# Optimization experiments

Measured on AMD Instinct MI355X. Metric: run time of the kernel, lower is better.

Reference implementation:

```python
import jax, jax.numpy as jnp
import numpy as np

CHUNK = 2048  # mirrors torch.chunk(pc, len(pc)//2048) with N a multiple of 2048


def _half(src, ref):
    """Faithful to the original: for each chunk of `src`, compute the
    [M, chunk] squared-distance matrix against `ref` and take min over the
    chunk axis (dim 1), yielding an M-vector per chunk; concatenate.
    Result shape: [num_chunks * M]."""
    chunks = src.reshape(-1, CHUNK, src.shape[-1])  # [num_chunks, CHUNK, 3]

    def per_chunk(chunk):
        diff = ref[:, None, :] - chunk[None, :, :]          # [M, CHUNK, 3]
        d = jnp.square(jnp.sqrt(jnp.sum(diff * diff, -1)))  # norm(...)**2
        return jnp.min(d, axis=1)                           # [M]

    return jax.lax.map(per_chunk, chunks).reshape(-1)


def setup_inputs() -> dict:
    key = jax.random.key(0)
    k1, k2 = jax.random.split(key)
    output_pc = jax.random.normal(k1, (1, 16384, 3), dtype=jnp.float32)
    gt_pc = jax.random.normal(k2, (1, 16384, 3), dtype=jnp.float32)
    return {"output_pc": output_pc, "gt_pc": gt_pc}


def reference(output_pc, gt_pc):
    pc1 = jnp.squeeze(output_pc)  # [N, 3]
    pc2 = jnp.squeeze(gt_pc)      # [M, 3]
    dist1 = _half(pc1, pc2)       # [ (N//CHUNK) * M ]
    dist2 = _half(pc2, pc1)       # [ (M//CHUNK) * N ]
    return jnp.mean(dist1) + jnp.mean(dist2)
```

## Files before the change

### kernel.cpp

```cpp
#include <hip/hip_runtime.h>
#include <float.h>

#define CHUNK 2048
#define SUB   2048
#define MBLK  128
#define GRP   256
#define NGRP  (SUB / GRP)

typedef __attribute__((ext_vector_type(8)))  short short8;
typedef __attribute__((ext_vector_type(16))) float f32x16;

static __device__ __forceinline__ unsigned short f2bf(float f) {
    unsigned u = __float_as_uint(f);
    return (unsigned short)((u + 0x7FFFu + ((u >> 16) & 1u)) >> 16);
}
static __device__ __forceinline__ float bf2f(unsigned short s) {
    return __uint_as_float(((unsigned)s) << 16);
}

static __device__ __forceinline__ void gld16(const void* g, void* l) {
    __builtin_amdgcn_global_load_lds(
        (const __attribute__((address_space(1))) void*)g,
        (__attribute__((address_space(3))) void*)l, 16, 0, 0);
}

__global__ void pack_kernel(const float* __restrict__ p1,
                            const float* __restrict__ p2, int n1, int n2,
                            unsigned short* __restrict__ Arec,
                            unsigned short* __restrict__ Brec)
{
    int i = blockIdx.x * blockDim.x + threadIdx.x;
    if (i >= n1 + n2) return;
    const bool isA = (i < n1);
    const float* s = isA ? p1 : p2;
    const int j = isA ? i : i - n1;
    float x = s[3 * j + 0], y = s[3 * j + 1], z = s[3 * j + 2];

    short8 lo, hi;
    if (isA) {
        unsigned short hx = f2bf(x), hy = f2bf(y), hz = f2bf(z);
        unsigned short lx = f2bf(x - bf2f(hx)), ly = f2bf(y - bf2f(hy)),
                       lz = f2bf(z - bf2f(hz));
        float sp = fmaf(x, x, fmaf(y, y, z * z));
        unsigned short sh = f2bf(sp), sl = f2bf(sp - bf2f(sh));
        lo[0]=(short)hx; lo[1]=(short)hy; lo[2]=(short)hz;
        lo[3]=(short)lx; lo[4]=(short)ly; lo[5]=(short)lz;
        lo[6]=(short)hx; lo[7]=(short)hy;
        hi[0]=(short)hz; hi[1]=(short)lx; hi[2]=(short)ly; hi[3]=(short)lz;
        hi[4]=(short)sh; hi[5]=(short)sl; hi[6]=(short)0x3F80; hi[7]=(short)0x3F80;
        short8* dst = (short8*)(Arec + (size_t)j * 16);
        dst[0] = lo; dst[1] = hi;
    } else {
        float ux = -2.0f * x, uy = -2.0f * y, uz = -2.0f * z;
        unsigned short hx = f2bf(ux), hy = f2bf(uy), hz = f2bf(uz);
        unsigned short lx = f2bf(ux - bf2f(hx)), ly = f2bf(uy - bf2f(hy)),
                       lz = f2bf(uz - bf2f(hz));
        float sq = fmaf(x, x, fmaf(y, y, z * z));
        unsigned short sh = f2bf(sq), sl = f2bf(sq - bf2f(sh));
        lo[0]=(short)hx; lo[1]=(short)hy; lo[2]=(short)hz;
        lo[3]=(short)hx; lo[4]=(short)hy; lo[5]=(short)hz;
        lo[6]=(short)lx; lo[7]=(short)ly;
        hi[0]=(short)lz; hi[1]=(short)lx; hi[2]=(short)ly; hi[3]=(short)lz;
        hi[4]=(short)0x3F80; hi[5]=(short)0x3F80; hi[6]=(short)sh; hi[7]=(short)sl;
        short8* dst = (short8*)(Brec + (size_t)j * 16);
        dst[0] = lo; dst[1] = hi;
    }
}

static __device__ __forceinline__ float tourney16(float rm[16], int l31)
{
#pragma unroll
    for (int r = 0; r < 8; ++r) {
        float lo = fminf(rm[r],     __shfl_xor(rm[r],     16));
        float hi = fminf(rm[r + 8], __shfl_xor(rm[r + 8], 16));
        rm[r] = (l31 & 16) ? hi : lo;
    }
#pragma unroll
    for (int r = 0; r < 4; ++r) {
        float lo = fminf(rm[r],     __shfl_xor(rm[r],     8));
        float hi = fminf(rm[r + 4], __shfl_xor(rm[r + 4], 8));
        rm[r] = (l31 & 8) ? hi : lo;
    }
#pragma unroll
    for (int r = 0; r < 2; ++r) {
        float lo = fminf(rm[r],     __shfl_xor(rm[r],     4));
        float hi = fminf(rm[r + 2], __shfl_xor(rm[r + 2], 4));
        rm[r] = (l31 & 4) ? hi : lo;
    }
    {
        float lo = fminf(rm[0], __shfl_xor(rm[0], 2));
        float hi = fminf(rm[1], __shfl_xor(rm[1], 2));
        rm[0] = (l31 & 2) ? hi : lo;
    }
    return fminf(rm[0], __shfl_xor(rm[0], 1));
}

__global__ __launch_bounds__(256, 8)
void chamfer_mfma(const unsigned short* __restrict__ Arec,
                  const unsigned short* __restrict__ Brec,
                  float* __restrict__ bsum,
                  int n1, int n2, float s2, float s1)
{
    __shared__ alignas(16) unsigned short sb[2][GRP * 16];
    __shared__ float wred[4];

    const int dir = blockIdx.z;
    const unsigned short* __restrict__ Ap = dir ? Brec : Arec;
    const unsigned short* __restrict__ Bp = dir ? Arec : Brec;
    const float scale = dir ? s1 : s2;
    const int rows_n = dir ? n2 : n1;
    const int cols_n = dir ? n1 : n2;

    const int tid  = threadIdx.x;
    const int g    = blockIdx.x;
    const int yb   = blockIdx.y;
    const int bid  = g + gridDim.x * (yb + gridDim.y * dir);
    if (g * MBLK >= rows_n || yb * SUB >= cols_n) {
        if (tid == 0) bsum[bid] = 0.0f;
        return;
    }

    const int lane = tid & 63;
    const int w    = tid >> 6;
    const int half = lane >> 5;
    const int l31  = lane & 31;

    const int rA = g * MBLK + w * 32 + l31;
    short8 aA = *(const short8*)(Ap + (size_t)rA * 16 + half * 8);

    const char* Bbytes = (const char*)(Bp + (size_t)(yb * SUB) * 16);

    const unsigned su = (unsigned)tid ^ (((unsigned)tid >> 3) & 7u);

    float rm[16];
#pragma unroll
    for (int r = 0; r < 16; ++r) rm[r] = FLT_MAX;
    const f32x16 z16 = {0,0,0,0, 0,0,0,0, 0,0,0,0, 0,0,0,0};

    {
        const char* gp = Bbytes + su * 16;
        char* lp = (char*)&sb[0][0] + w * 1024;
        gld16(gp, lp);
        gld16(gp + 4096, lp + 4096);
    }
    __syncthreads();

    const unsigned ru = (((unsigned)(l31 * 2 + half)) ^ ((unsigned)l31 >> 2)) * 8u;

    for (int gr = 0; gr < NGRP; ++gr) {
        const int cur = gr & 1;
        if (gr + 1 < NGRP) {
            const char* gp = Bbytes + (size_t)(gr + 1) * 8192 + su * 16;
            char* lp = (char*)&sb[cur ^ 1][0] + w * 1024;
            gld16(gp, lp);
            gld16(gp + 4096, lp + 4096);
        }
        const unsigned short* lb = &sb[cur][ru];
#pragma unroll
        for (int tt = 0; tt < GRP / 32; ++tt) {
            short8 b = *(const short8*)(lb + (size_t)tt * 512);
            f32x16 d = __builtin_amdgcn_mfma_f32_32x32x16_bf16(aA, b, z16, 0, 0, 0);
#pragma unroll
            for (int r = 0; r < 16; ++r) rm[r] = fminf(rm[r], d[r]);
        }
        __syncthreads();
    }

    float v = tourney16(rm, l31);
    float c = ((l31 & 1) == 0) ? fmaxf(v, 0.0f) : 0.0f;
#pragma unroll
    for (int off = 32; off > 0; off >>= 1) c += __shfl_down(c, off);
    if (lane == 0) wred[w] = c;
    __syncthreads();
    if (tid == 0)
        bsum[bid] = (wred[0] + wred[1] + wred[2] + wred[3]) * scale;
}

__global__ __launch_bounds__(256)
void final_reduce(const float* __restrict__ bsum, float* __restrict__ out, int n)
{
    __shared__ float wred[4];
    float s = 0.0f;
    for (int i = threadIdx.x; i < n; i += 256) s += bsum[i];
#pragma unroll
    for (int off = 32; off > 0; off >>= 1) s += __shfl_down(s, off);
    const int lane = threadIdx.x & 63, w = threadIdx.x >> 6;
    if (lane == 0) wred[w] = s;
    __syncthreads();
    if (threadIdx.x == 0)
        out[0] = wred[0] + wred[1] + wred[2] + wred[3];
}

#define FB_RPT  2
#define FB_TILE (256 * FB_RPT)
__global__ __launch_bounds__(256, 2)
void chamfer_valu(const float* __restrict__ p1, const float* __restrict__ p2,
                  int n1, int n2, float* __restrict__ out)
{
    __shared__ float4 q[CHUNK];
    __shared__ float wsum[4];
    const int dir = blockIdx.z;
    const float* __restrict__ src = dir ? p2 : p1;
    const float* __restrict__ ref = dir ? p1 : p2;
    const int nsrc = dir ? n2 : n1;
    const int m    = dir ? n1 : n2;
    const int nchunks = nsrc / CHUNK;
    const int c = blockIdx.y;
    const int tile0 = blockIdx.x * FB_TILE;
    if (c >= nchunks || tile0 >= m) return;
    const float scale = 1.0f / ((float)nchunks * (float)m);
    const float* __restrict__ chunk = src + (size_t)c * CHUNK * 3;
    for (int k = threadIdx.x; k < CHUNK; k += 256) {
        float x = chunk[3*k], y = chunk[3*k+1], z = chunk[3*k+2];
        q[k] = make_float4(x, y, z, fmaf(x, x, fmaf(y, y, z * z)));
    }
    __syncthreads();
    float px[FB_RPT], py[FB_RPT], pz[FB_RPT], sp[FB_RPT], mna[FB_RPT], mnb[FB_RPT];
    bool valid[FB_RPT];
#pragma unroll
    for (int r = 0; r < FB_RPT; ++r) {
        int j = tile0 + threadIdx.x + r * 256;
        valid[r] = (j < m);
        int jj = valid[r] ? j : 0;
        float x = ref[3*jj], y = ref[3*jj+1], z = ref[3*jj+2];
        px[r] = -2.0f*x; py[r] = -2.0f*y; pz[r] = -2.0f*z;
        sp[r] = fmaf(x, x, fmaf(y, y, z * z));
        mna[r] = FLT_MAX; mnb[r] = FLT_MAX;
    }
#pragma unroll 2
    for (int k = 0; k < CHUNK; k += 2) {
        float4 qa = q[k], qb = q[k+1];
#pragma unroll
        for (int r = 0; r < FB_RPT; ++r) {
            mna[r] = fminf(mna[r], fmaf(px[r], qa.x, fmaf(py[r], qa.y, fmaf(pz[r], qa.z, qa.w))));
            mnb[r] = fminf(mnb[r], fmaf(px[r], qb.x, fmaf(py[r], qb.y, fmaf(pz[r], qb.z, qb.w))));
        }
    }
    float sum = 0.0f;
#pragma unroll
    for (int r = 0; r < FB_RPT; ++r)
        if (valid[r]) sum += fmaxf(fminf(mna[r], mnb[r]) + sp[r], 0.0f);
#pragma unroll
    for (int off = 32; off > 0; off >>= 1) sum += __shfl_down(sum, off);
    if ((threadIdx.x & 63) == 0) wsum[threadIdx.x >> 6] = sum;
    __syncthreads();
    if (threadIdx.x == 0)
        atomicAdd(out, (wsum[0]+wsum[1]+wsum[2]+wsum[3]) * scale);
}

extern "C" void kernel_launch(void* const* d_in, const int* in_sizes, int n_in,
                              void* d_out, int out_size, void* d_ws, size_t ws_size,
                              hipStream_t stream)
{
    const float* p1 = (const float*)d_in[0];
    const float* p2 = (const float*)d_in[1];
    float* out = (float*)d_out;
    const int n1 = in_sizes[0] / 3;
    const int n2 = in_sizes[1] / 3;

    const int nc1 = n1 / CHUNK, nc2 = n2 / CHUNK;

    const int gx = max(n1, n2) / MBLK;
    const int gy = max(n1, n2) / SUB;
    const int nblocks = gx * gy * 2;

    unsigned short* Arec = (unsigned short*)d_ws;
    unsigned short* Brec = Arec + (size_t)n1 * 16;
    float* bsum = (float*)(Brec + (size_t)n2 * 16);
    const size_t need = (size_t)(n1 + n2) * 32 + (size_t)nblocks * 4;

    const bool shapes_ok = (n1 % CHUNK == 0) && (n2 % CHUNK == 0) &&
                           (n1 % MBLK == 0) && (n2 % MBLK == 0) &&
                           (n1 % SUB == 0) && (n2 % SUB == 0);

    if (shapes_ok && ws_size >= need) {
        pack_kernel<<<(n1 + n2 + 255) / 256, 256, 0, stream>>>(
            p1, p2, n1, n2, Arec, Brec);
        dim3 grid(gx, gy, 2);
        chamfer_mfma<<<grid, 256, 0, stream>>>(
            Arec, Brec, bsum, n1, n2,
            1.0f / ((float)nc2 * (float)n1), 1.0f / ((float)nc1 * (float)n2));
        final_reduce<<<1, 256, 0, stream>>>(bsum, out, nblocks);
    } else {
        const int t1 = (n2 + FB_TILE - 1) / FB_TILE;
        const int t2 = (n1 + FB_TILE - 1) / FB_TILE;
        dim3 grid(max(t1, t2), max(nc1, nc2), 2);
        chamfer_valu<<<grid, 256, 0, stream>>>(p1, p2, n1, n2, out);
    }
}
```

Before: 82.92 us.

## Fuse bf16 split packing into chamfer kernel, drop separate pack kernel

Removes the standalone pack kernel and its workspace round trip. Each block now reads raw float xyz points, packs the A-row fragment in registers, and packs B columns on the fly into swizzled LDS double buffers. The next group's global loads are issued before the MFMA loop and packed after it. This saves one kernel launch and the global write/read of packed records, at the cost of redundant packing across blocks and extra VALU work in the main loop.

```diff
diff --git a/kernel.cpp b/kernel.cpp
--- a/kernel.cpp
+++ b/kernel.cpp
@@ -18,53 +18,40 @@
     return __uint_as_float(((unsigned)s) << 16);
 }
 
-static __device__ __forceinline__ void gld16(const void* g, void* l) {
-    __builtin_amdgcn_global_load_lds(
-        (const __attribute__((address_space(1))) void*)g,
-        (__attribute__((address_space(3))) void*)l, 16, 0, 0);
-}
-
-__global__ void pack_kernel(const float* __restrict__ p1,
-                            const float* __restrict__ p2, int n1, int n2,
-                            unsigned short* __restrict__ Arec,
-                            unsigned short* __restrict__ Brec)
-{
-    int i = blockIdx.x * blockDim.x + threadIdx.x;
-    if (i >= n1 + n2) return;
-    const bool isA = (i < n1);
-    const float* s = isA ? p1 : p2;
-    const int j = isA ? i : i - n1;
-    float x = s[3 * j + 0], y = s[3 * j + 1], z = s[3 * j + 2];
-
-    short8 lo, hi;
-    if (isA) {
-        unsigned short hx = f2bf(x), hy = f2bf(y), hz = f2bf(z);
-        unsigned short lx = f2bf(x - bf2f(hx)), ly = f2bf(y - bf2f(hy)),
-                       lz = f2bf(z - bf2f(hz));
-        float sp = fmaf(x, x, fmaf(y, y, z * z));
-        unsigned short sh = f2bf(sp), sl = f2bf(sp - bf2f(sh));
-        lo[0]=(short)hx; lo[1]=(short)hy; lo[2]=(short)hz;
-        lo[3]=(short)lx; lo[4]=(short)ly; lo[5]=(short)lz;
-        lo[6]=(short)hx; lo[7]=(short)hy;
-        hi[0]=(short)hz; hi[1]=(short)lx; hi[2]=(short)ly; hi[3]=(short)lz;
-        hi[4]=(short)sh; hi[5]=(short)sl; hi[6]=(short)0x3F80; hi[7]=(short)0x3F80;
-        short8* dst = (short8*)(Arec + (size_t)j * 16);
-        dst[0] = lo; dst[1] = hi;
+static __device__ __forceinline__ short8 packA_half(float x, float y, float z,
+                                                    int half)
+{
+    unsigned short hx = f2bf(x), hy = f2bf(y), hz = f2bf(z);
+    unsigned short lx = f2bf(x - bf2f(hx)), ly = f2bf(y - bf2f(hy)),
+                   lz = f2bf(z - bf2f(hz));
+    float sp = fmaf(x, x, fmaf(y, y, z * z));
+    unsigned short sh = f2bf(sp), sl = f2bf(sp - bf2f(sh));
+    short8 a;
+    if (half == 0) {
+        a[0]=(short)hx; a[1]=(short)hy; a[2]=(short)hz;
+        a[3]=(short)lx; a[4]=(short)ly; a[5]=(short)lz;
+        a[6]=(short)hx; a[7]=(short)hy;
     } else {
-        float ux = -2.0f * x, uy = -2.0f * y, uz = -2.0f * z;
-        unsigned short hx = f2bf(ux), hy = f2bf(uy), hz = f2bf(uz);
-        unsigned short lx = f2bf(ux - bf2f(hx)), ly = f2bf(uy - bf2f(hy)),
-                       lz = f2bf(uz - bf2f(hz));
-        float sq = fmaf(x, x, fmaf(y, y, z * z));
-        unsigned short sh = f2bf(sq), sl = f2bf(sq - bf2f(sh));
-        lo[0]=(short)hx; lo[1]=(short)hy; lo[2]=(short)hz;
-        lo[3]=(short)hx; lo[4]=(short)hy; lo[5]=(short)hz;
-        lo[6]=(short)lx; lo[7]=(short)ly;
-        hi[0]=(short)lz; hi[1]=(short)lx; hi[2]=(short)ly; hi[3]=(short)lz;
-        hi[4]=(short)0x3F80; hi[5]=(short)0x3F80; hi[6]=(short)sh; hi[7]=(short)sl;
-        short8* dst = (short8*)(Brec + (size_t)j * 16);
-        dst[0] = lo; dst[1] = hi;
-    }
+        a[0]=(short)hz; a[1]=(short)lx; a[2]=(short)ly; a[3]=(short)lz;
+        a[4]=(short)sh; a[5]=(short)sl; a[6]=(short)0x3F80; a[7]=(short)0x3F80;
+    }
+    return a;
+}
+
+static __device__ __forceinline__ void packB_halves(float x, float y, float z,
+                                                    short8& lo, short8& hi)
+{
+    float ux = -2.0f * x, uy = -2.0f * y, uz = -2.0f * z;
+    unsigned short hx = f2bf(ux), hy = f2bf(uy), hz = f2bf(uz);
+    unsigned short lx = f2bf(ux - bf2f(hx)), ly = f2bf(uy - bf2f(hy)),
+                   lz = f2bf(uz - bf2f(hz));
+    float sq = fmaf(x, x, fmaf(y, y, z * z));
+    unsigned short sh = f2bf(sq), sl = f2bf(sq - bf2f(sh));
+    lo[0]=(short)hx; lo[1]=(short)hy; lo[2]=(short)hz;
+    lo[3]=(short)hx; lo[4]=(short)hy; lo[5]=(short)hz;
+    lo[6]=(short)lx; lo[7]=(short)ly;
+    hi[0]=(short)lz; hi[1]=(short)lx; hi[2]=(short)ly; hi[3]=(short)lz;
+    hi[4]=(short)0x3F80; hi[5]=(short)0x3F80; hi[6]=(short)sh; hi[7]=(short)sl;
 }
 
 static __device__ __forceinline__ float tourney16(float rm[16], int l31)
@@ -96,8 +83,7 @@
 }
 
 __global__ __launch_bounds__(256, 8)
-void chamfer_mfma(const unsigned short* __restrict__ Arec,
-                  const unsigned short* __restrict__ Brec,
+void chamfer_mfma(const float* __restrict__ p1, const float* __restrict__ p2,
                   float* __restrict__ bsum,
                   int n1, int n2, float s2, float s1)
 {
@@ -105,8 +91,8 @@
     __shared__ float wred[4];
 
     const int dir = blockIdx.z;
-    const unsigned short* __restrict__ Ap = dir ? Brec : Arec;
-    const unsigned short* __restrict__ Bp = dir ? Arec : Brec;
+    const float* __restrict__ Asrc = dir ? p2 : p1;
+    const float* __restrict__ Bsrc = dir ? p1 : p2;
     const float scale = dir ? s1 : s2;
     const int rows_n = dir ? n2 : n1;
     const int cols_n = dir ? n1 : n2;
@@ -126,34 +112,36 @@
     const int l31  = lane & 31;
 
     const int rA = g * MBLK + w * 32 + l31;
-    short8 aA = *(const short8*)(Ap + (size_t)rA * 16 + half * 8);
-
-    const char* Bbytes = (const char*)(Bp + (size_t)(yb * SUB) * 16);
-
-    const unsigned su = (unsigned)tid ^ (((unsigned)tid >> 3) & 7u);
+    const float* ap = Asrc + 3 * (size_t)rA;
+    short8 aA = packA_half(ap[0], ap[1], ap[2], half);
+
+    const float* __restrict__ bp = Bsrc + 3 * (size_t)(yb * SUB);
+
+    const unsigned wm  = ((unsigned)tid >> 2) & 7u;
+    const unsigned wu0 = ((2u * (unsigned)tid)      ^ wm) * 8u;
+    const unsigned wu1 = ((2u * (unsigned)tid + 1u) ^ wm) * 8u;
+    const unsigned ru  = (((unsigned)(l31 * 2 + half)) ^ ((unsigned)l31 >> 2)) * 8u;
 
     float rm[16];
 #pragma unroll
     for (int r = 0; r < 16; ++r) rm[r] = FLT_MAX;
     const f32x16 z16 = {0,0,0,0, 0,0,0,0, 0,0,0,0, 0,0,0,0};
 
+    float nx, ny, nz;
+    { const float* q = bp + 3 * (size_t)tid; nx = q[0]; ny = q[1]; nz = q[2]; }
     {
-        const char* gp = Bbytes + su * 16;
-        char* lp = (char*)&sb[0][0] + w * 1024;
-        gld16(gp, lp);
-        gld16(gp + 4096, lp + 4096);
-    }
-    __syncthreads();
-
-    const unsigned ru = (((unsigned)(l31 * 2 + half)) ^ ((unsigned)l31 >> 2)) * 8u;
+        short8 lo, hi;
+        packB_halves(nx, ny, nz, lo, hi);
+        *(short8*)&sb[0][wu0] = lo;
+        *(short8*)&sb[0][wu1] = hi;
+    }
+    __syncthreads();
 
     for (int gr = 0; gr < NGRP; ++gr) {
         const int cur = gr & 1;
         if (gr + 1 < NGRP) {
-            const char* gp = Bbytes + (size_t)(gr + 1) * 8192 + su * 16;
-            char* lp = (char*)&sb[cur ^ 1][0] + w * 1024;
-            gld16(gp, lp);
-            gld16(gp + 4096, lp + 4096);
+            const float* q = bp + 3 * (size_t)((gr + 1) * GRP + tid);
+            nx = q[0]; ny = q[1]; nz = q[2];
         }
         const unsigned short* lb = &sb[cur][ru];
 #pragma unroll
@@ -162,6 +150,12 @@
             f32x16 d = __builtin_amdgcn_mfma_f32_32x32x16_bf16(aA, b, z16, 0, 0, 0);
 #pragma unroll
             for (int r = 0; r < 16; ++r) rm[r] = fminf(rm[r], d[r]);
+        }
+        if (gr + 1 < NGRP) {
+            short8 lo, hi;
+            packB_halves(nx, ny, nz, lo, hi);
+            *(short8*)&sb[cur ^ 1][wu0] = lo;
+            *(short8*)&sb[cur ^ 1][wu1] = hi;
         }
         __syncthreads();
     }
@@ -264,21 +258,17 @@
     const int gy = max(n1, n2) / SUB;
     const int nblocks = gx * gy * 2;
 
-    unsigned short* Arec = (unsigned short*)d_ws;
-    unsigned short* Brec = Arec + (size_t)n1 * 16;
-    float* bsum = (float*)(Brec + (size_t)n2 * 16);
-    const size_t need = (size_t)(n1 + n2) * 32 + (size_t)nblocks * 4;
+    float* bsum = (float*)d_ws;
+    const size_t need = (size_t)nblocks * 4;
 
     const bool shapes_ok = (n1 % CHUNK == 0) && (n2 % CHUNK == 0) &&
                            (n1 % MBLK == 0) && (n2 % MBLK == 0) &&
                            (n1 % SUB == 0) && (n2 % SUB == 0);
 
     if (shapes_ok && ws_size >= need) {
-        pack_kernel<<<(n1 + n2 + 255) / 256, 256, 0, stream>>>(
-            p1, p2, n1, n2, Arec, Brec);
         dim3 grid(gx, gy, 2);
         chamfer_mfma<<<grid, 256, 0, stream>>>(
-            Arec, Brec, bsum, n1, n2,
+            p1, p2, bsum, n1, n2,
             1.0f / ((float)nc2 * (float)n1), 1.0f / ((float)nc1 * (float)n2));
         final_reduce<<<1, 256, 0, stream>>>(bsum, out, nblocks);
     } else {
```

After: 86.52 us. 1.04x slower.
